# Kernel tuning notes

Measured on AMD Instinct MI355X. Metric: run time of the kernel, lower is better.

Reference implementation:

```python
import jax, jax.numpy as jnp
import numpy as np

B, S, DMODEL, HEADS = 2, 2048, 1024, 16
DK = DMODEL // HEADS
DV = DMODEL // HEADS


def setup_inputs() -> dict:
    key = jax.random.key(0)
    kx, kq, kk, kv = jax.random.split(key, 4)
    x = jax.random.normal(kx, (B, S, DMODEL), dtype=jnp.float32)
    # stacked per-head projection weights, shape [H, dmodel, dk/dv]
    # (equivalent to nn.Linear(dmodel, dk, bias=False) per head)
    scale = 1.0 / np.sqrt(DMODEL)
    Wq = jax.random.uniform(kq, (HEADS, DMODEL, DK), jnp.float32, -scale, scale)
    Wk = jax.random.uniform(kk, (HEADS, DMODEL, DK), jnp.float32, -scale, scale)
    Wv = jax.random.uniform(kv, (HEADS, DMODEL, DV), jnp.float32, -scale, scale)
    return {"x": x, "Wq": Wq, "Wk": Wk, "Wv": Wv}


def reference(x, Wq, Wk, Wv):
    # per-head projections, batched across heads: [B,H,S,dk]
    q = jnp.einsum("bsd,hdk->bhsk", x, Wq)
    k = jnp.einsum("bsd,hdk->bhsk", x, Wk)
    v = jnp.einsum("bsd,hdv->bhsv", x, Wv)
    # NOTE: original module applies NO 1/sqrt(dk) scaling — keep faithful
    scores = jnp.einsum("bhqk,bhsk->bhqs", q, k)  # [B,H,S,S]
    attn = jax.nn.softmax(scores, axis=-1)
    out = jnp.einsum("bhqs,bhsv->bhqv", attn, v)  # [B,H,S,dv]
    # concat heads along last dim in head order
    Bsz, H, Sq, Dv = out.shape
    return jnp.transpose(out, (0, 2, 1, 3)).reshape(Bsz, Sq, H * Dv)
```

## Files before the change

### kernel.cpp

```cpp
#include <hip/hip_runtime.h>

#define B_ 2
#define S_ 2048
#define D_ 1024
#define H_ 16
#define DK_ 64
#define M_ (B_ * S_)
#define N_ (3 * D_)

typedef __bf16 bf16x8 __attribute__((ext_vector_type(8)));
typedef short s8vec __attribute__((ext_vector_type(8)));
typedef float f4vec __attribute__((ext_vector_type(4)));

static __device__ __forceinline__ ushort f2b(float f) {
  union { float f; unsigned u; } v; v.f = f;
  unsigned u = v.u;
  u += 0x7FFFu + ((u >> 16) & 1u);
  return (ushort)(u >> 16);
}

static __device__ __forceinline__ unsigned pk2(float a, float b) {
#if __has_builtin(__builtin_amdgcn_cvt_pk_bf16_f32)
  typedef __bf16 b2 __attribute__((ext_vector_type(2)));
  b2 r = __builtin_amdgcn_cvt_pk_bf16_f32(a, b);
  return __builtin_bit_cast(unsigned, r);
#else
  return (unsigned)f2b(a) | ((unsigned)f2b(b) << 16);
#endif
}

static __device__ __forceinline__ f4vec mfma16(s8vec a, s8vec b, f4vec c) {
  return __builtin_amdgcn_mfma_f32_16x16x32_bf16(
      __builtin_bit_cast(bf16x8, a), __builtin_bit_cast(bf16x8, b), c, 0, 0, 0);
}

static __device__ __forceinline__ void gl_lds16(const ushort* g, ushort* l) {
  __builtin_amdgcn_global_load_lds(
      (const __attribute__((address_space(1))) unsigned*)g,
      (__attribute__((address_space(3))) unsigned*)l, 16, 0, 0);
}

__global__ void cvt_x(const float* __restrict__ x, ushort* __restrict__ xb) {
  int i = blockIdx.x * 256 + threadIdx.x;
  float4 v = ((const float4*)x)[i];
  ushort4 o;
  o.x = f2b(v.x); o.y = f2b(v.y); o.z = f2b(v.z); o.w = f2b(v.w);
  ((ushort4*)xb)[i] = o;
}

__global__ __launch_bounds__(256) void cvt_w(const float* __restrict__ Wq,
                                             const float* __restrict__ Wk,
                                             const float* __restrict__ Wv,
                                             ushort* __restrict__ wbt) {
  __shared__ ushort T[64 * 72];
  const int w = blockIdx.z, h = blockIdx.y, d0 = blockIdx.x * 64;
  const float* W = (w == 0) ? Wq : (w == 1) ? Wk : Wv;
  const float* src = W + (size_t)h * 65536 + (size_t)d0 * 64;
  const int t = threadIdx.x;
#pragma unroll
  for (int j = 0; j < 4; ++j) {
    int idx = j * 256 + t;
    int dr = idx >> 4, kc = (idx & 15) * 4;
    float4 v = *(const float4*)(src + dr * 64 + kc);
    T[(kc + 0) * 72 + dr] = f2b(v.x);
    T[(kc + 1) * 72 + dr] = f2b(v.y);
    T[(kc + 2) * 72 + dr] = f2b(v.z);
    T[(kc + 3) * 72 + dr] = f2b(v.w);
  }
  __syncthreads();
  const int kk = t >> 2, dcg = (t & 3) * 16;
  ushort* dst = wbt + ((size_t)w * 1024 + h * 64 + kk) * 1024 + d0 + dcg;
  *(s8vec*)dst       = *(const s8vec*)&T[kk * 72 + dcg];
  *(s8vec*)(dst + 8) = *(const s8vec*)&T[kk * 72 + dcg + 8];
}

__global__ __launch_bounds__(256) void proj_gemm(const ushort* __restrict__ xb,
                                                 const ushort* __restrict__ wbt,
                                                 ushort* __restrict__ qkv) {
  __shared__ __attribute__((aligned(16))) ushort As[128 * 64];
  __shared__ __attribute__((aligned(16))) ushort Bs[128 * 64];
  const int tid = threadIdx.x, wid = tid >> 6, lane = tid & 63;
  const int quad = lane >> 4, l15 = lane & 15;
  const int wm = wid & 1, wn = wid >> 1;
  const int m0 = blockIdx.x * 128, n0 = blockIdx.y * 128;

  f4vec acc[4][4];
#pragma unroll
  for (int mb = 0; mb < 4; mb++)
#pragma unroll
    for (int nb = 0; nb < 4; nb++)
#pragma unroll
      for (int i = 0; i < 4; i++) acc[mb][nb][i] = 0.f;

  const int sr = tid >> 3, sg = tid & 7;
  const int lg = sg ^ (sr & 7);
  const ushort* Ab = xb + (size_t)m0 * D_;
  const ushort* Bb = wbt + (size_t)n0 * D_;

  for (int k0 = 0; k0 < D_; k0 += 64) {
    __syncthreads();
#pragma unroll
    for (int j = 0; j < 4; ++j) {
      int r = j * 32 + sr;
      gl_lds16(Ab + (size_t)r * D_ + k0 + lg * 8, &As[j * 2048 + wid * 512]);
      gl_lds16(Bb + (size_t)r * D_ + k0 + lg * 8, &Bs[j * 2048 + wid * 512]);
    }
    __syncthreads();

#pragma unroll
    for (int kb = 0; kb < 2; ++kb) {
      s8vec af[4], bf[4];
#pragma unroll
      for (int mb = 0; mb < 4; ++mb) {
        int m = wm * 64 + mb * 16 + l15;
        int gpos = (kb * 4 + quad) ^ (m & 7);
        af[mb] = *(const s8vec*)&As[m * 64 + gpos * 8];
      }
#pragma unroll
      for (int nb = 0; nb < 4; ++nb) {
        int n = wn * 64 + nb * 16 + l15;
        int gpos = (kb * 4 + quad) ^ (n & 7);
        bf[nb] = *(const s8vec*)&Bs[n * 64 + gpos * 8];
      }
#pragma unroll
      for (int mb = 0; mb < 4; ++mb)
#pragma unroll
        for (int nb = 0; nb < 4; ++nb)
          acc[mb][nb] = mfma16(af[mb], bf[nb], acc[mb][nb]);
    }
  }

  const size_t per = (size_t)B_ * H_ * S_ * DK_;
  const int w = n0 >> 10;
  if (w == 2) {
    ushort* vt = qkv + 2 * per;
#pragma unroll
    for (int mb = 0; mb < 4; ++mb)
#pragma unroll
      for (int nb = 0; nb < 4; ++nb)
#pragma unroll
        for (int i = 0; i < 4; ++i) {
          int m = m0 + wm * 64 + mb * 16 + quad * 4 + i;
          int b = m >> 11, s = m & 2047;
          int n1 = (n0 & 1023) + wn * 64 + nb * 16 + l15;
          vt[((size_t)b * 1024 + n1) * S_ + s] = f2b(acc[mb][nb][i]);
        }
  } else {
#pragma unroll
    for (int mb = 0; mb < 4; ++mb)
#pragma unroll
      for (int nb = 0; nb < 4; ++nb)
#pragma unroll
        for (int i = 0; i < 4; ++i) {
          int m = m0 + wm * 64 + mb * 16 + quad * 4 + i;
          int b = m >> 11, s = m & 2047;
          int n1 = (n0 & 1023) + wn * 64 + nb * 16 + l15;
          qkv[(size_t)w * per + (((size_t)b * H_ + (n1 >> 6)) * S_ + s) * 64 + (n1 & 63)] =
              f2b(acc[mb][nb][i]);
        }
  }
}

__global__ __launch_bounds__(512) void attn(const ushort* __restrict__ qg,
                                            const ushort* __restrict__ kg,
                                            const ushort* __restrict__ vtg,
                                            float* __restrict__ out) {
  __shared__ __attribute__((aligned(16))) ushort Ks[64 * 64];
  __shared__ __attribute__((aligned(16))) ushort Vt[64 * 64];
  __shared__ __attribute__((aligned(16))) ushort Ps[8][16 * 76];
  const int qt = blockIdx.x, bh = blockIdx.y;
  const int b = bh >> 4, h = bh & 15;
  const int tid = threadIdx.x, wid = tid >> 6, lane = tid & 63;
  const int quad = lane >> 4, l15 = lane & 15;

  const ushort* qbase = qg + ((size_t)bh * S_ + qt * 128 + wid * 16) * DK_;
  s8vec aq0 = *(const s8vec*)(qbase + (size_t)l15 * DK_ + quad * 8);
  s8vec aq1 = *(const s8vec*)(qbase + (size_t)l15 * DK_ + 32 + quad * 8);

  f4vec o[4];
  float lsum[4];
#pragma unroll
  for (int i = 0; i < 4; i++) {
    lsum[i] = 0.f;
#pragma unroll
    for (int nb = 0; nb < 4; nb++) o[nb][i] = 0.f;
  }

  const int srow = wid * 8 + (lane >> 3);
  const int lg = (lane & 7) ^ (lane >> 3);
  ushort* ksdst = &Ks[wid * 512];
  ushort* vtdst = &Vt[wid * 512];
  const ushort* kb_ = kg + (size_t)bh * S_ * DK_;
  const ushort* vb_ = vtg + (size_t)bh * 64 * S_;
  const int l7 = l15 & 7;

  for (int kt = 0; kt < S_ / 64; ++kt) {
    __syncthreads();
    gl_lds16(kb_ + ((size_t)(kt * 64 + srow)) * DK_ + lg * 8, ksdst);
    gl_lds16(vb_ + (size_t)srow * S_ + kt * 64 + lg * 8, vtdst);
    __syncthreads();

    f4vec sc[4];
#pragma unroll
    for (int nb = 0; nb < 4; nb++) {
#pragma unroll
      for (int i = 0; i < 4; i++) sc[nb][i] = 0.f;
      s8vec bk0 = *(const s8vec*)&Ks[(nb * 16 + l15) * 64 + ((0 * 4 + quad) ^ l7) * 8];
      s8vec bk1 = *(const s8vec*)&Ks[(nb * 16 + l15) * 64 + ((1 * 4 + quad) ^ l7) * 8];
      sc[nb] = mfma16(aq0, bk0, sc[nb]);
      sc[nb] = mfma16(aq1, bk1, sc[nb]);
    }

#pragma unroll
    for (int nb = 0; nb < 4; nb++) {
#pragma unroll
      for (int i = 0; i < 4; i++) {
        float p = __expf(sc[nb][i]);
        sc[nb][i] = p;
        lsum[i] += p;
      }
      unsigned p01 = pk2(sc[nb][0], sc[nb][1]);
      unsigned p23 = pk2(sc[nb][2], sc[nb][3]);
      ushort* pw = &Ps[wid][quad * 4 * 76 + nb * 16 + l15];
      pw[0]   = (ushort)p01;
      pw[76]  = (ushort)(p01 >> 16);
      pw[152] = (ushort)p23;
      pw[228] = (ushort)(p23 >> 16);
    }

#pragma unroll
    for (int kb2 = 0; kb2 < 2; kb2++) {
      s8vec ap = *(const s8vec*)(&Ps[wid][l15 * 76 + kb2 * 32 + quad * 8]);
#pragma unroll
      for (int nb = 0; nb < 4; nb++) {
        s8vec bv = *(const s8vec*)&Vt[(nb * 16 + l15) * 64 + ((kb2 * 4 + quad) ^ l7) * 8];
        o[nb] = mfma16(ap, bv, o[nb]);
      }
    }
  }

#pragma unroll
  for (int i = 0; i < 4; i++) {
#pragma unroll
    for (int msk = 1; msk < 16; msk <<= 1) lsum[i] += __shfl_xor(lsum[i], msk, 64);
  }

  float* ob = out + ((size_t)b * S_ + qt * 128 + wid * 16) * D_ + h * DK_;
#pragma unroll
  for (int i = 0; i < 4; i++) {
    float inv = 1.0f / lsum[i];
#pragma unroll
    for (int nb = 0; nb < 4; nb++)
      ob[(size_t)(quad * 4 + i) * D_ + nb * 16 + l15] = o[nb][i] * inv;
  }
}

extern "C" void kernel_launch(void* const* d_in, const int* in_sizes, int n_in,
                              void* d_out, int out_size, void* d_ws, size_t ws_size,
                              hipStream_t stream) {
  const float* x  = (const float*)d_in[0];
  const float* Wq = (const float*)d_in[1];
  const float* Wk = (const float*)d_in[2];
  const float* Wv = (const float*)d_in[3];
  float* out = (float*)d_out;

  ushort* xb  = (ushort*)d_ws;
  ushort* wbt = xb + (size_t)B_ * S_ * D_;
  ushort* qkv = wbt + (size_t)3 * D_ * D_;
  const size_t per = (size_t)B_ * H_ * S_ * DK_;

  cvt_x<<<(B_ * S_ * D_) / 4 / 256, 256, 0, stream>>>(x, xb);
  cvt_w<<<dim3(16, 16, 3), 256, 0, stream>>>(Wq, Wk, Wv, wbt);
  proj_gemm<<<dim3(M_ / 128, N_ / 128), 256, 0, stream>>>(xb, wbt, qkv);
  attn<<<dim3(S_ / 128, B_ * H_), 512, 0, stream>>>(qkv, qkv + per, qkv + 2 * per, out);
}
```

Measured before the change: 179.7 us.

## Double-tile KV loop to 128 keys with register-prefetched next tile

The attention kernel now processes 128 keys per iteration instead of 64, halving the number of barrier pairs. K and V^T tiles are loaded into registers one iteration ahead and stored to LDS after the barrier, replacing the direct global-to-LDS loads so global latency overlaps the MFMA and exp work. A custom barrier waits only on LDS counters so the outstanding global prefetch is not drained. The cost is more registers and a larger LDS footprint (bigger P buffer), which may reduce occupancy.

Result: faster. 175.2 us (-2.5%).

```diff
diff --git a/kernel.cpp b/kernel.cpp
--- a/kernel.cpp
+++ b/kernel.cpp
@@ -38,6 +38,13 @@
   __builtin_amdgcn_global_load_lds(
       (const __attribute__((address_space(1))) unsigned*)g,
       (__attribute__((address_space(3))) unsigned*)l, 16, 0, 0);
+}
+
+static __device__ __forceinline__ void wg_barrier_lds() {
+  asm volatile("" ::: "memory");
+  __builtin_amdgcn_s_waitcnt(0xC07F);
+  __builtin_amdgcn_s_barrier();
+  asm volatile("" ::: "memory");
 }
 
 __global__ void cvt_x(const float* __restrict__ x, ushort* __restrict__ xb) {
@@ -165,13 +172,13 @@
                                             const ushort* __restrict__ kg,
                                             const ushort* __restrict__ vtg,
                                             float* __restrict__ out) {
-  __shared__ __attribute__((aligned(16))) ushort Ks[64 * 64];
-  __shared__ __attribute__((aligned(16))) ushort Vt[64 * 64];
-  __shared__ __attribute__((aligned(16))) ushort Ps[8][16 * 76];
+  __shared__ __attribute__((aligned(16))) ushort Ks[128 * 64];
+  __shared__ __attribute__((aligned(16))) ushort Vt[2][64 * 64];
+  __shared__ __attribute__((aligned(16))) ushort Ps[8][16 * 132];
   const int qt = blockIdx.x, bh = blockIdx.y;
   const int b = bh >> 4, h = bh & 15;
   const int tid = threadIdx.x, wid = tid >> 6, lane = tid & 63;
-  const int quad = lane >> 4, l15 = lane & 15;
+  const int quad = lane >> 4, l15 = lane & 15, l7 = l15 & 7;
 
   const ushort* qbase = qg + ((size_t)bh * S_ + qt * 128 + wid * 16) * DK_;
   s8vec aq0 = *(const s8vec*)(qbase + (size_t)l15 * DK_ + quad * 8);
@@ -186,33 +193,46 @@
     for (int nb = 0; nb < 4; nb++) o[nb][i] = 0.f;
   }
 
-  const int srow = wid * 8 + (lane >> 3);
-  const int lg = (lane & 7) ^ (lane >> 3);
-  ushort* ksdst = &Ks[wid * 512];
-  ushort* vtdst = &Vt[wid * 512];
+  const int r = tid >> 3, gs = tid & 7;
+  const int gk = gs ^ (r & 7);
   const ushort* kb_ = kg + (size_t)bh * S_ * DK_;
-  const ushort* vb_ = vtg + (size_t)bh * 64 * S_;
-  const int l7 = l15 & 7;
-
-  for (int kt = 0; kt < S_ / 64; ++kt) {
-    __syncthreads();
-    gl_lds16(kb_ + ((size_t)(kt * 64 + srow)) * DK_ + lg * 8, ksdst);
-    gl_lds16(vb_ + (size_t)srow * S_ + kt * 64 + lg * 8, vtdst);
-    __syncthreads();
-
-    f4vec sc[4];
-#pragma unroll
-    for (int nb = 0; nb < 4; nb++) {
+  const ushort* vb_ = vtg + (size_t)bh * 64 * S_ + (size_t)r * S_;
+
+  s8vec kr0 = *(const s8vec*)(kb_ + (size_t)r * DK_ + gk * 8);
+  s8vec kr1 = *(const s8vec*)(kb_ + (size_t)(64 + r) * DK_ + gk * 8);
+  s8vec vr0 = *(const s8vec*)(vb_ + gk * 8);
+  s8vec vr1 = *(const s8vec*)(vb_ + 64 + gk * 8);
+
+  for (int kt = 0; kt < S_ / 128; ++kt) {
+    wg_barrier_lds();
+    *(s8vec*)&Ks[r * 64 + gs * 8]        = kr0;
+    *(s8vec*)&Ks[(64 + r) * 64 + gs * 8] = kr1;
+    *(s8vec*)&Vt[0][r * 64 + gs * 8]     = vr0;
+    *(s8vec*)&Vt[1][r * 64 + gs * 8]     = vr1;
+    if (kt + 1 < S_ / 128) {
+      const ushort* kn = kb_ + (size_t)((kt + 1) * 128 + r) * DK_ + gk * 8;
+      kr0 = *(const s8vec*)(kn);
+      kr1 = *(const s8vec*)(kn + (size_t)64 * DK_);
+      const ushort* vn = vb_ + (kt + 1) * 128 + gk * 8;
+      vr0 = *(const s8vec*)(vn);
+      vr1 = *(const s8vec*)(vn + 64);
+    }
+    wg_barrier_lds();
+
+    f4vec sc[8];
+#pragma unroll
+    for (int nb = 0; nb < 8; nb++) {
 #pragma unroll
       for (int i = 0; i < 4; i++) sc[nb][i] = 0.f;
-      s8vec bk0 = *(const s8vec*)&Ks[(nb * 16 + l15) * 64 + ((0 * 4 + quad) ^ l7) * 8];
-      s8vec bk1 = *(const s8vec*)&Ks[(nb * 16 + l15) * 64 + ((1 * 4 + quad) ^ l7) * 8];
+      const int row = nb * 16 + l15;
+      s8vec bk0 = *(const s8vec*)&Ks[row * 64 + ((0 + quad) ^ l7) * 8];
+      s8vec bk1 = *(const s8vec*)&Ks[row * 64 + ((4 + quad) ^ l7) * 8];
       sc[nb] = mfma16(aq0, bk0, sc[nb]);
       sc[nb] = mfma16(aq1, bk1, sc[nb]);
     }
 
 #pragma unroll
-    for (int nb = 0; nb < 4; nb++) {
+    for (int nb = 0; nb < 8; nb++) {
 #pragma unroll
       for (int i = 0; i < 4; i++) {
         float p = __expf(sc[nb][i]);
@@ -221,19 +241,20 @@
       }
       unsigned p01 = pk2(sc[nb][0], sc[nb][1]);
       unsigned p23 = pk2(sc[nb][2], sc[nb][3]);
-      ushort* pw = &Ps[wid][quad * 4 * 76 + nb * 16 + l15];
+      ushort* pw = &Ps[wid][quad * 4 * 132 + nb * 16 + l15];
       pw[0]   = (ushort)p01;
-      pw[76]  = (ushort)(p01 >> 16);
-      pw[152] = (ushort)p23;
-      pw[228] = (ushort)(p23 >> 16);
-    }
-
-#pragma unroll
-    for (int kb2 = 0; kb2 < 2; kb2++) {
-      s8vec ap = *(const s8vec*)(&Ps[wid][l15 * 76 + kb2 * 32 + quad * 8]);
+      pw[132] = (ushort)(p01 >> 16);
+      pw[264] = (ushort)p23;
+      pw[396] = (ushort)(p23 >> 16);
+    }
+
+#pragma unroll
+    for (int kb2 = 0; kb2 < 4; kb2++) {
+      s8vec ap = *(const s8vec*)(&Ps[wid][l15 * 132 + kb2 * 32 + quad * 8]);
+      const int half = kb2 >> 1, G = (kb2 & 1) * 4 + quad;
 #pragma unroll
       for (int nb = 0; nb < 4; nb++) {
-        s8vec bv = *(const s8vec*)&Vt[(nb * 16 + l15) * 64 + ((kb2 * 4 + quad) ^ l7) * 8];
+        s8vec bv = *(const s8vec*)&Vt[half][(nb * 16 + l15) * 64 + (G ^ l7) * 8];
         o[nb] = mfma16(ap, bv, o[nb]);
       }
     }
```
